# Kernel optimization log

Hardware: AMD Instinct MI355X
Metric: run time of the kernel (lower is better)

## Reference

```python
import jax, jax.numpy as jnp
import numpy as np

N, A, B, K = 100000, 64, 128, 27  # active sites, in/out channels, 3^3 offsets
EPS = 1e-4  # scn BatchNorm default eps
LEAK = 0.0  # leakiness=0 -> ReLU


def bn_lrelu(x, gamma, beta):
    # training-mode BN over active sites, fused leaky relu
    mu = x.mean(0)
    var = x.var(0)
    xh = (x - mu) * jax.lax.rsqrt(var + EPS) * gamma + beta
    return jnp.where(xh > 0, xh, LEAK * xh)


def subconv(f, nbr, mask, W):
    # submanifold conv via rulebook: f [N,Cin], nbr [N,K], mask [N,K], W [K,Cin,Cout]
    out = jnp.zeros((f.shape[0], W.shape[2]), f.dtype)
    for k in range(W.shape[0]):  # fixed small set of kernel offsets
        g = jnp.where(mask[:, k:k + 1], f[nbr[:, k]], jnp.zeros((), f.dtype))
        out = out + g @ W[k]
    return out


def setup_inputs() -> dict:
    key = jax.random.key(0)
    ks = jax.random.split(key, 8)
    feat = jax.random.normal(ks[0], (N, A), jnp.float32)
    nbr = jax.random.randint(ks[1], (N, K), 0, N, jnp.int32)
    mask = jax.random.randint(ks[2], (N, K), 0, 2, jnp.int32).astype(bool)
    # self-connection at center offset is always valid in submanifold conv
    center = K // 2
    nbr = nbr.at[:, center].set(jnp.arange(N, dtype=jnp.int32))
    mask = mask.at[:, center].set(True)
    s1 = 1.0 / np.sqrt(K * A)
    s2 = 1.0 / np.sqrt(K * B)
    W1 = jax.random.normal(ks[3], (K, A, B), jnp.float32) * s1
    W2 = jax.random.normal(ks[4], (K, B, B), jnp.float32) * s2
    Wnin = jax.random.normal(ks[5], (A, B), jnp.float32) / np.sqrt(A)
    gamma1 = jnp.ones((A,), jnp.float32)
    beta1 = jnp.zeros((A,), jnp.float32)
    gamma2 = jnp.ones((B,), jnp.float32)
    beta2 = jnp.zeros((B,), jnp.float32)
    return {"feat": feat, "gamma1": gamma1, "beta1": beta1, "W1": W1,
            "gamma2": gamma2, "beta2": beta2, "W2": W2, "Wnin": Wnin,
            "nbr": nbr, "mask": mask}


def reference(feat, gamma1, beta1, W1, gamma2, beta2, W2, Wnin, nbr, mask):
    y1 = feat @ Wnin  # NetworkInNetwork shortcut (a != b)
    h = bn_lrelu(feat, gamma1, beta1)
    h = subconv(h, nbr, mask, W1)
    h = bn_lrelu(h, gamma2, beta2)
    y2 = subconv(h, nbr, mask, W2)
    return y1 + y2  # add_feature_planes
```

## Files before the change

### kernel.cpp

```cpp
#include <hip/hip_runtime.h>
#include <stdint.h>

#define CA 64
#define CB 128
#define KOFF 27
#define BN_EPS 1e-4f

typedef short bf16x8 __attribute__((ext_vector_type(8)));
typedef float f32x4 __attribute__((ext_vector_type(4)));
typedef unsigned int u32x4 __attribute__((ext_vector_type(4)));
typedef unsigned short u16x4 __attribute__((ext_vector_type(4)));

__device__ __forceinline__ unsigned short f2bf(float f) {
  union { float f; uint32_t u; } c; c.f = f;
  uint32_t u = c.u;
  return (unsigned short)((u + 0x7FFFu + ((u >> 16) & 1u)) >> 16);
}

__device__ __forceinline__ void barrier_lds() {
  asm volatile("s_waitcnt lgkmcnt(0)\n\ts_barrier" ::: "memory");
}

__global__ void detect_mask_k(const unsigned char* __restrict__ m, int* flag) {
  unsigned v = 0;
  for (int i = threadIdx.x; i < 4096; i += 256)
    if (i & 3) v |= m[i];
  if (v) atomicOr(flag, 1);
}

__global__ void pack_mask_k(const void* __restrict__ mp, const int* __restrict__ flag,
                            uint32_t* __restrict__ bits, int n) {
  int i = blockIdx.x * blockDim.x + threadIdx.x;
  if (i >= n) return;
  uint32_t b = 0;
  if (*flag) {
    const unsigned char* m = (const unsigned char*)mp + (size_t)i * KOFF;
    for (int k = 0; k < KOFF; k++) b |= (m[k] ? 1u : 0u) << k;
  } else {
    const int* m = (const int*)mp + (size_t)i * KOFF;
    for (int k = 0; k < KOFF; k++) b |= (m[k] ? 1u : 0u) << k;
  }
  bits[i] = b;
}

__global__ void transpose_all_k(const float* __restrict__ W1, const float* __restrict__ W2,
                                const float* __restrict__ Wnin,
                                unsigned short* __restrict__ w1t, unsigned short* __restrict__ w2t,
                                unsigned short* __restrict__ wnt) {
  const int t1 = KOFF * CA * CB, t2 = KOFF * CB * CB, t3 = CA * CB;
  int idx = blockIdx.x * blockDim.x + threadIdx.x;
  if (idx < t1) {
    int ci = idx % CA; int r = idx / CA; int co = r % CB; int k = r / CB;
    w1t[idx] = f2bf(W1[((size_t)k * CA + ci) * CB + co]);
  } else if (idx < t1 + t2) {
    int j = idx - t1;
    int ci = j % CB; int r = j / CB; int co = r % CB; int k = r / CB;
    w2t[j] = f2bf(W2[((size_t)k * CB + ci) * CB + co]);
  } else if (idx < t1 + t2 + t3) {
    int j = idx - t1 - t2;
    int ci = j % CA; int co = j / CA;
    wnt[j] = f2bf(Wnin[(size_t)ci * CB + co]);
  }
}

template<int C>
__global__ void col_stats_k(const float* __restrict__ x, int n, float* __restrict__ sums) {
  __shared__ float ssum[C], ssq[C];
  int t = threadIdx.x;
  for (int i = t; i < C; i += 256) { ssum[i] = 0.f; ssq[i] = 0.f; }
  __syncthreads();
  const int c = t % C;
  const int rpb = 256 / C;
  float s = 0.f, q = 0.f;
  for (int r = blockIdx.x * rpb + t / C; r < n; r += gridDim.x * rpb) {
    float v = x[(size_t)r * C + c];
    s += v; q += v * v;
  }
  atomicAdd(&ssum[c], s);
  atomicAdd(&ssq[c], q);
  __syncthreads();
  for (int i = t; i < C; i += 256) {
    atomicAdd(&sums[i], ssum[i]);
    atomicAdd(&sums[C + i], ssq[i]);
  }
}

template<int C>
__global__ void bn_finalize_k(const float* __restrict__ sums, const float* __restrict__ gamma,
                              const float* __restrict__ beta, float* __restrict__ sc, int n) {
  int c = threadIdx.x;
  if (c >= C) return;
  float inv_n = 1.f / (float)n;
  float mean = sums[c] * inv_n;
  float var = sums[C + c] * inv_n - mean * mean;
  float rstd = rsqrtf(var + BN_EPS);
  float scale = gamma[c] * rstd;
  sc[c] = scale;
  sc[C + c] = beta[c] - mean * scale;
}

template<int C, bool RAW>
__global__ void bn_apply_k(const float* __restrict__ x, const float* __restrict__ sc,
                           unsigned short* __restrict__ h, unsigned short* __restrict__ raw,
                           int total) {
  int idx = (blockIdx.x * blockDim.x + threadIdx.x) * 4;
  if (idx >= total) return;
  f32x4 v = *(const f32x4*)&x[idx];
  int c0 = idx % C;
  u16x4 ho, ro;
#pragma unroll
  for (int j = 0; j < 4; j++) {
    float s = sc[c0 + j], b = sc[C + c0 + j];
    float hv = fmaxf(v[j] * s + b, 0.f);
    ho[j] = f2bf(hv);
    if (RAW) ro[j] = f2bf(v[j]);
  }
  *(u16x4*)&h[idx] = ho;
  if (RAW) *(u16x4*)&raw[idx] = ro;
}

template<int CIN, bool FUSE, bool STATS>
__launch_bounds__(256, 4)
__global__ void conv_k(const unsigned short* __restrict__ hin,
                       const unsigned short* __restrict__ wt,
                       const int* __restrict__ nbr,
                       const uint32_t* __restrict__ mbits,
                       const unsigned short* __restrict__ fbraw,
                       const unsigned short* __restrict__ wnt,
                       float* __restrict__ out, float* __restrict__ sums, int n) {
  constexpr int TR = 64;
  constexpr int NKS = CIN / 32;
  constexpr int CH = CIN / 8;
  constexpr int RPP = 256 / CH;
  constexpr int NP = TR / RPP;

  __shared__ alignas(16) unsigned short tile[2][TR * CIN];
  __shared__ int lnbr[TR * KOFF];
  __shared__ uint32_t lmb[TR];

  const int t = threadIdx.x;
  const int rowbase = blockIdx.x * TR;
  const int nrows = min(TR, n - rowbase);

  for (int i = t; i < nrows * KOFF; i += 256)
    lnbr[i] = nbr[(size_t)rowbase * KOFF + i] * (CIN * 2);
  if (t < TR) lmb[t] = (t < nrows) ? mbits[rowbase + t] : 0u;
  barrier_lds();

  const int lane = t & 63;
  const int wave = t >> 6;
  const int l16 = lane & 15;
  const int quad = lane >> 4;
  const int colbase = wave * 32;
  const int c16 = t % CH;
  const int grow = t / CH;
  const int boff0 = (colbase + l16) * CIN + quad * 8;
  const int boff1 = boff0 + 16 * CIN;

  int toff[NP]; int pnb[NP]; uint32_t pmb[NP];
#pragma unroll
  for (int p = 0; p < NP; p++) {
    int r = p * RPP + grow;
    toff[p] = r * CIN + ((c16 ^ (r & (CH - 1))) * 8);
    pnb[p] = r * KOFF;
    pmb[p] = lmb[r];
  }

  f32x4 acc[4][2];
#pragma unroll
  for (int i = 0; i < 4; i++) { acc[i][0] = f32x4{0,0,0,0}; acc[i][1] = f32x4{0,0,0,0}; }

  bf16x8 bfr[2 * NKS];
  u32x4 gr[2][NP];
  u32x4 g0[NP];

#define LOADB(kk, dst)                                                         \
  {                                                                            \
    const unsigned short* wk = wt + (size_t)(kk) * (CB * CIN);                 \
    _Pragma("unroll")                                                          \
    for (int ks = 0; ks < NKS; ks++) {                                         \
      dst[2 * ks]     = *(const bf16x8*)&wk[boff0 + ks * 32];                  \
      dst[2 * ks + 1] = *(const bf16x8*)&wk[boff1 + ks * 32];                  \
    }                                                                          \
  }

#define GATHER(kk, dst)                                                        \
  {                                                                            \
    _Pragma("unroll")                                                          \
    for (int p = 0; p < NP; p++) {                                             \
      u32x4 v = {0, 0, 0, 0};                                                  \
      if ((pmb[p] >> (kk)) & 1u)                                               \
        v = *(const u32x4*)((const char*)hin +                                 \
                            (size_t)(unsigned)lnbr[pnb[p] + (kk)] + c16 * 16); \
      dst[p] = v;                                                              \
    }                                                                          \
  }

#define STAGE(buf, src)                                                        \
  {                                                                            \
    _Pragma("unroll")                                                          \
    for (int p = 0; p < NP; p++) *(u32x4*)&tile[buf][toff[p]] = src[p];        \
  }

#define MMA(buf)                                                               \
  {                                                                            \
    _Pragma("unroll")                                                          \
    for (int ks = 0; ks < NKS; ks++) {                                         \
      _Pragma("unroll")                                                        \
      for (int rt = 0; rt < 4; rt++) {                                         \
        int row = rt * 16 + l16;                                               \
        bf16x8 a = *(const bf16x8*)&tile[buf][row * CIN +                      \
                      (((ks * 4 + quad) ^ (row & (CH - 1))) * 8)];             \
        acc[rt][0] = __builtin_amdgcn_mfma_f32_16x16x32_bf16(a, bfr[2 * ks],     acc[rt][0], 0, 0, 0); \
        acc[rt][1] = __builtin_amdgcn_mfma_f32_16x16x32_bf16(a, bfr[2 * ks + 1], acc[rt][1], 0, 0, 0); \
      }                                                                        \
    }                                                                          \
  }

  LOADB(0, bfr);
  GATHER(0, g0);

  if constexpr (FUSE) {
#pragma unroll
    for (int ks = 0; ks < CA / 32; ks++) {
      bf16x8 b0 = *(const bf16x8*)&wnt[(colbase + l16) * CA + ks * 32 + quad * 8];
      bf16x8 b1 = *(const bf16x8*)&wnt[(colbase + 16 + l16) * CA + ks * 32 + quad * 8];
#pragma unroll
      for (int rt = 0; rt < 4; rt++) {
        int r = rt * 16 + l16;
        bf16x8 a = bf16x8{0, 0, 0, 0, 0, 0, 0, 0};
        if (r < nrows)
          a = *(const bf16x8*)&fbraw[(size_t)(rowbase + r) * CA + ks * 32 + quad * 8];
        acc[rt][0] = __builtin_amdgcn_mfma_f32_16x16x32_bf16(a, b0, acc[rt][0], 0, 0, 0);
        acc[rt][1] = __builtin_amdgcn_mfma_f32_16x16x32_bf16(a, b1, acc[rt][1], 0, 0, 0);
      }
    }
  }

  STAGE(0, g0);
  GATHER(1, gr[0]);
  GATHER(2, gr[1]);
  barrier_lds();

#pragma unroll
  for (int k = 0; k < KOFF; k++) {
    const int cur = k & 1, nxt = cur ^ 1;
    MMA(cur);
    if (k + 1 < KOFF) {
      LOADB(k + 1, bfr);
      STAGE(nxt, gr[cur]);
      if (k + 3 < KOFF) GATHER(k + 3, gr[cur]);
      barrier_lds();
    }
  }
#undef LOADB
#undef GATHER
#undef STAGE
#undef MMA

#pragma unroll
  for (int rt = 0; rt < 4; rt++) {
#pragma unroll
    for (int ct = 0; ct < 2; ct++) {
#pragma unroll
      for (int i = 0; i < 4; i++) {
        int r = rt * 16 + quad * 4 + i;
        if (r < nrows) {
          int c = colbase + ct * 16 + l16;
          out[(size_t)(rowbase + r) * CB + c] = acc[rt][ct][i];
        }
      }
    }
  }

  if constexpr (STATS) {
#pragma unroll
    for (int ct = 0; ct < 2; ct++) {
      float s = 0.f, q = 0.f;
#pragma unroll
      for (int rt = 0; rt < 4; rt++)
#pragma unroll
        for (int i = 0; i < 4; i++) { float v = acc[rt][ct][i]; s += v; q += v * v; }
      s += __shfl_xor(s, 16); s += __shfl_xor(s, 32);
      q += __shfl_xor(q, 16); q += __shfl_xor(q, 32);
      if (quad == 0) {
        int cch = colbase + ct * 16 + l16;
        atomicAdd(&sums[cch], s);
        atomicAdd(&sums[CB + cch], q);
      }
    }
  }
}

extern "C" void kernel_launch(void* const* d_in, const int* in_sizes, int n_in,
                              void* d_out, int out_size, void* d_ws, size_t ws_size,
                              hipStream_t stream) {
  const float* feat   = (const float*)d_in[0];
  const float* gamma1 = (const float*)d_in[1];
  const float* beta1  = (const float*)d_in[2];
  const float* W1     = (const float*)d_in[3];
  const float* gamma2 = (const float*)d_in[4];
  const float* beta2  = (const float*)d_in[5];
  const float* W2     = (const float*)d_in[6];
  const float* Wnin   = (const float*)d_in[7];
  const int*   nbr    = (const int*)d_in[8];
  const void*  mask   = d_in[9];
  float* out = (float*)d_out;

  const int n = in_sizes[0] / CA;

  char* ws = (char*)d_ws;
  size_t off = 0;
  auto alloc = [&](size_t bytes) { size_t p = off; off += (bytes + 255) & ~(size_t)255; return p; };
  int*            flag  = (int*)           (ws + alloc(256));
  float*          sums1 = (float*)         (ws + alloc(2 * CA * 4));
  float*          sums2 = (float*)         (ws + alloc(2 * CB * 4));
  float*          sc1   = (float*)         (ws + alloc(2 * CA * 4));
  float*          sc2   = (float*)         (ws + alloc(2 * CB * 4));
  uint32_t*       mbits = (uint32_t*)      (ws + alloc((size_t)n * 4));
  unsigned short* fb    = (unsigned short*)(ws + alloc((size_t)n * CA * 2));
  unsigned short* hb1   = (unsigned short*)(ws + alloc((size_t)n * CA * 2));
  float*          out1  = (float*)         (ws + alloc((size_t)n * CB * 4));
  unsigned short* hb2   = (unsigned short*)(ws + alloc((size_t)n * CB * 2));
  unsigned short* w1t   = (unsigned short*)(ws + alloc((size_t)KOFF * CB * CA * 2));
  unsigned short* w2t   = (unsigned short*)(ws + alloc((size_t)KOFF * CB * CB * 2));
  unsigned short* wnt   = (unsigned short*)(ws + alloc((size_t)CB * CA * 2));

  hipMemsetAsync(d_ws, 0, 1792, stream);

  detect_mask_k<<<1, 256, 0, stream>>>((const unsigned char*)mask, flag);
  pack_mask_k<<<(n + 255) / 256, 256, 0, stream>>>(mask, flag, mbits, n);

  {
    int tot = KOFF * CA * CB + KOFF * CB * CB + CA * CB;
    transpose_all_k<<<(tot + 255) / 256, 256, 0, stream>>>(W1, W2, Wnin, w1t, w2t, wnt);
  }

  col_stats_k<CA><<<256, 256, 0, stream>>>(feat, n, sums1);
  bn_finalize_k<CA><<<1, CA, 0, stream>>>(sums1, gamma1, beta1, sc1, n);
  bn_apply_k<CA, true><<<(n * CA / 4 + 255) / 256, 256, 0, stream>>>(feat, sc1, hb1, fb, n * CA);

  conv_k<CA, false, true><<<(n + 63) / 64, 256, 0, stream>>>(hb1, w1t, nbr, mbits, nullptr, nullptr, out1, sums2, n);

  bn_finalize_k<CB><<<1, CB, 0, stream>>>(sums2, gamma2, beta2, sc2, n);
  bn_apply_k<CB, false><<<(n * CB / 4 + 255) / 256, 256, 0, stream>>>(out1, sc2, hb2, nullptr, n * CB);

  conv_k<CB, true, false><<<(n + 63) / 64, 256, 0, stream>>>(hb2, w2t, nbr, mbits, fb, wnt, out, nullptr, n);
}
```

Measured before the change: 536.4 us.

## Gather conv A-operands directly from global into registers, dropping LDS staging

Replaces the LDS double-buffered gather tile and barriers with per-lane direct global loads of the neighbour rows in MFMA operand layout. The neighbour indices are read from global per offset and a two-deep register pipeline covers latency. The launch-bounds occupancy hint is removed. This eliminates LDS writes, reads and block-wide barriers. In exchange each wave issues its own redundant gathers, four waves reloading the same rows, so L2 traffic rises, and register pressure may change occupancy.

```diff
diff --git a/kernel.cpp b/kernel.cpp
--- a/kernel.cpp
+++ b/kernel.cpp
@@ -15,10 +15,6 @@
   union { float f; uint32_t u; } c; c.f = f;
   uint32_t u = c.u;
   return (unsigned short)((u + 0x7FFFu + ((u >> 16) & 1u)) >> 16);
-}
-
-__device__ __forceinline__ void barrier_lds() {
-  asm volatile("s_waitcnt lgkmcnt(0)\n\ts_barrier" ::: "memory");
 }
 
 __global__ void detect_mask_k(const unsigned char* __restrict__ m, int* flag) {
@@ -120,7 +116,7 @@
 }
 
 template<int CIN, bool FUSE, bool STATS>
-__launch_bounds__(256, 4)
+__launch_bounds__(256)
 __global__ void conv_k(const unsigned short* __restrict__ hin,
                        const unsigned short* __restrict__ wt,
                        const int* __restrict__ nbr,
@@ -130,95 +126,79 @@
                        float* __restrict__ out, float* __restrict__ sums, int n) {
   constexpr int TR = 64;
   constexpr int NKS = CIN / 32;
-  constexpr int CH = CIN / 8;
-  constexpr int RPP = 256 / CH;
-  constexpr int NP = TR / RPP;
-
-  __shared__ alignas(16) unsigned short tile[2][TR * CIN];
-  __shared__ int lnbr[TR * KOFF];
-  __shared__ uint32_t lmb[TR];
+  constexpr int NG = KOFF * NKS;
 
   const int t = threadIdx.x;
-  const int rowbase = blockIdx.x * TR;
-  const int nrows = min(TR, n - rowbase);
-
-  for (int i = t; i < nrows * KOFF; i += 256)
-    lnbr[i] = nbr[(size_t)rowbase * KOFF + i] * (CIN * 2);
-  if (t < TR) lmb[t] = (t < nrows) ? mbits[rowbase + t] : 0u;
-  barrier_lds();
-
   const int lane = t & 63;
   const int wave = t >> 6;
   const int l16 = lane & 15;
   const int quad = lane >> 4;
   const int colbase = wave * 32;
-  const int c16 = t % CH;
-  const int grow = t / CH;
-  const int boff0 = (colbase + l16) * CIN + quad * 8;
-  const int boff1 = boff0 + 16 * CIN;
-
-  int toff[NP]; int pnb[NP]; uint32_t pmb[NP];
-#pragma unroll
-  for (int p = 0; p < NP; p++) {
-    int r = p * RPP + grow;
-    toff[p] = r * CIN + ((c16 ^ (r & (CH - 1))) * 8);
-    pnb[p] = r * KOFF;
-    pmb[p] = lmb[r];
-  }
+  const int rowbase = blockIdx.x * TR;
+  const int nrows = min(TR, n - rowbase);
+
+  uint32_t pm[4];
+  int nbo[4];
+#pragma unroll
+  for (int rt = 0; rt < 4; rt++) {
+    int r = rt * 16 + l16;
+    bool ok = r < nrows;
+    pm[rt] = ok ? mbits[rowbase + r] : 0u;
+    nbo[rt] = (ok ? (rowbase + r) : rowbase) * KOFF;
+  }
+
+  const char* hq  = (const char*)hin + quad * 16;
+  const char* wq0 = (const char*)wt + ((colbase + l16) * CIN + quad * 8) * 2;
+  const char* wq1 = wq0 + 16 * CIN * 2;
 
   f32x4 acc[4][2];
 #pragma unroll
   for (int i = 0; i < 4; i++) { acc[i][0] = f32x4{0,0,0,0}; acc[i][1] = f32x4{0,0,0,0}; }
 
-  bf16x8 bfr[2 * NKS];
-  u32x4 gr[2][NP];
-  u32x4 g0[NP];
-
-#define LOADB(kk, dst)                                                         \
-  {                                                                            \
-    const unsigned short* wk = wt + (size_t)(kk) * (CB * CIN);                 \
+  int nb0[4], nb1[4], nb2[4];
+  bf16x8 aA[4], aB[4];
+  bf16x8 bA0, bA1, bB0, bB1;
+
+#define LDNB_BODY(kk, nb)                                                      \
+    { _Pragma("unroll")                                                        \
+      for (int rt = 0; rt < 4; rt++) nb[rt] = nbr[nbo[rt] + (kk)]; }
+#define LDNB(kk) do {                                                          \
+    if (((kk) % 3) == 0)      LDNB_BODY(kk, nb0)                               \
+    else if (((kk) % 3) == 1) LDNB_BODY(kk, nb1)                               \
+    else                      LDNB_BODY(kk, nb2)                               \
+  } while (0)
+
+#define LOADA_BODY(kk, ks, nb, a)                                              \
+    { _Pragma("unroll")                                                        \
+      for (int rt = 0; rt < 4; rt++) {                                         \
+        bf16x8 v = bf16x8{0, 0, 0, 0, 0, 0, 0, 0};                             \
+        if ((pm[rt] >> (kk)) & 1u)                                             \
+          v = *(const bf16x8*)(hq +                                            \
+                (size_t)((unsigned)nb[rt] * (unsigned)(CIN * 2)) + (ks) * 64); \
+        a[rt] = v; } }
+#define LOADA(kk, ks, a) do {                                                  \
+    if (((kk) % 3) == 0)      LOADA_BODY(kk, ks, nb0, a)                       \
+    else if (((kk) % 3) == 1) LOADA_BODY(kk, ks, nb1, a)                       \
+    else                      LOADA_BODY(kk, ks, nb2, a)                       \
+  } while (0)
+
+#define LOADW(kk, ks, b0, b1) do {                                             \
+    int woff = (kk) * (CB * CIN * 2) + (ks) * 64;                              \
+    b0 = *(const bf16x8*)(wq0 + woff);                                         \
+    b1 = *(const bf16x8*)(wq1 + woff);                                         \
+  } while (0)
+
+#define MMA8(a, b0, b1) do {                                                   \
     _Pragma("unroll")                                                          \
-    for (int ks = 0; ks < NKS; ks++) {                                         \
-      dst[2 * ks]     = *(const bf16x8*)&wk[boff0 + ks * 32];                  \
-      dst[2 * ks + 1] = *(const bf16x8*)&wk[boff1 + ks * 32];                  \
-    }                                                                          \
-  }
-
-#define GATHER(kk, dst)                                                        \
-  {                                                                            \
-    _Pragma("unroll")                                                          \
-    for (int p = 0; p < NP; p++) {                                             \
-      u32x4 v = {0, 0, 0, 0};                                                  \
-      if ((pmb[p] >> (kk)) & 1u)                                               \
-        v = *(const u32x4*)((const char*)hin +                                 \
-                            (size_t)(unsigned)lnbr[pnb[p] + (kk)] + c16 * 16); \
-      dst[p] = v;                                                              \
-    }                                                                          \
-  }
-
-#define STAGE(buf, src)                                                        \
-  {                                                                            \
-    _Pragma("unroll")                                                          \
-    for (int p = 0; p < NP; p++) *(u32x4*)&tile[buf][toff[p]] = src[p];        \
-  }
-
-#define MMA(buf)                                                               \
-  {                                                                            \
-    _Pragma("unroll")                                                          \
-    for (int ks = 0; ks < NKS; ks++) {                                         \
-      _Pragma("unroll")                                                        \
-      for (int rt = 0; rt < 4; rt++) {                                         \
-        int row = rt * 16 + l16;                                               \
-        bf16x8 a = *(const bf16x8*)&tile[buf][row * CIN +                      \
-                      (((ks * 4 + quad) ^ (row & (CH - 1))) * 8)];             \
-        acc[rt][0] = __builtin_amdgcn_mfma_f32_16x16x32_bf16(a, bfr[2 * ks],     acc[rt][0], 0, 0, 0); \
-        acc[rt][1] = __builtin_amdgcn_mfma_f32_16x16x32_bf16(a, bfr[2 * ks + 1], acc[rt][1], 0, 0, 0); \
-      }                                                                        \
-    }                                                                          \
-  }
-
-  LOADB(0, bfr);
-  GATHER(0, g0);
+    for (int rt = 0; rt < 4; rt++) {                                           \
+      acc[rt][0] = __builtin_amdgcn_mfma_f32_16x16x32_bf16(a[rt], b0, acc[rt][0], 0, 0, 0); \
+      acc[rt][1] = __builtin_amdgcn_mfma_f32_16x16x32_bf16(a[rt], b1, acc[rt][1], 0, 0, 0); \
+    } } while (0)
+
+  LDNB(0);
+  LDNB(1);
+  LOADA(0, 0, aA); LOADW(0, 0, bA0, bA1);
+  LOADA(0, 1, aB); LOADW(0, 1, bB0, bB1);
 
   if constexpr (FUSE) {
 #pragma unroll
@@ -237,26 +217,25 @@
     }
   }
 
-  STAGE(0, g0);
-  GATHER(1, gr[0]);
-  GATHER(2, gr[1]);
-  barrier_lds();
-
-#pragma unroll
-  for (int k = 0; k < KOFF; k++) {
-    const int cur = k & 1, nxt = cur ^ 1;
-    MMA(cur);
-    if (k + 1 < KOFF) {
-      LOADB(k + 1, bfr);
-      STAGE(nxt, gr[cur]);
-      if (k + 3 < KOFF) GATHER(k + 3, gr[cur]);
-      barrier_lds();
+#pragma unroll
+  for (int g = 0; g < NG; g++) {
+    const int k = g / NKS, ks = g % NKS;
+    (void)ks;
+    if ((g & 1) == 0) MMA8(aA, bA0, bA1); else MMA8(aB, bB0, bB1);
+    if ((g % NKS) == 0 && k + 2 < KOFF) LDNB(k + 2);
+    const int g2 = g + 2;
+    if (g2 < NG) {
+      const int k2 = g2 / NKS, ks2 = g2 % NKS;
+      if ((g & 1) == 0) { LOADA(k2, ks2, aA); LOADW(k2, ks2, bA0, bA1); }
+      else              { LOADA(k2, ks2, aB); LOADW(k2, ks2, bB0, bB1); }
     }
   }
-#undef LOADB
-#undef GATHER
-#undef STAGE
-#undef MMA
+#undef LDNB_BODY
+#undef LDNB
+#undef LOADA_BODY
+#undef LOADA
+#undef LOADW
+#undef MMA8
 
 #pragma unroll
   for (int rt = 0; rt < 4; rt++) {
```

New measurement: 851.8 us. 58.8% more time.

## Gather neighbor rows directly into LDS with global_load_lds DMA

Applied to the files above, without the earlier changes.

Replaces the register-staged gather (global load to VGPRs, then store to LDS) with global_load_lds direct-to-LDS transfers. Masked-off neighbors read from a zeroed scratch page. Neighbor indices are loaded per offset from global memory into registers instead of being prestaged in LDS. The swizzle moves into the source address, and barriers now wait on vmcnt so the next offset's DMA overlaps the current MMA. This removes VGPR traffic and the LDS prologue, but leaves only one offset of prefetch depth instead of two, and drops the launch-bounds occupancy hint.

```diff
diff --git a/kernel.cpp b/kernel.cpp
--- a/kernel.cpp
+++ b/kernel.cpp
@@ -15,10 +15,6 @@
   union { float f; uint32_t u; } c; c.f = f;
   uint32_t u = c.u;
   return (unsigned short)((u + 0x7FFFu + ((u >> 16) & 1u)) >> 16);
-}
-
-__device__ __forceinline__ void barrier_lds() {
-  asm volatile("s_waitcnt lgkmcnt(0)\n\ts_barrier" ::: "memory");
 }
 
 __global__ void detect_mask_k(const unsigned char* __restrict__ m, int* flag) {
@@ -120,59 +116,72 @@
 }
 
 template<int CIN, bool FUSE, bool STATS>
-__launch_bounds__(256, 4)
+__launch_bounds__(256)
 __global__ void conv_k(const unsigned short* __restrict__ hin,
                        const unsigned short* __restrict__ wt,
                        const int* __restrict__ nbr,
                        const uint32_t* __restrict__ mbits,
                        const unsigned short* __restrict__ fbraw,
                        const unsigned short* __restrict__ wnt,
+                       const char* __restrict__ zpage,
                        float* __restrict__ out, float* __restrict__ sums, int n) {
   constexpr int TR = 64;
   constexpr int NKS = CIN / 32;
   constexpr int CH = CIN / 8;
   constexpr int RPP = 256 / CH;
+  constexpr int RPW = 64 / CH;
   constexpr int NP = TR / RPP;
 
   __shared__ alignas(16) unsigned short tile[2][TR * CIN];
-  __shared__ int lnbr[TR * KOFF];
-  __shared__ uint32_t lmb[TR];
 
   const int t = threadIdx.x;
-  const int rowbase = blockIdx.x * TR;
-  const int nrows = min(TR, n - rowbase);
-
-  for (int i = t; i < nrows * KOFF; i += 256)
-    lnbr[i] = nbr[(size_t)rowbase * KOFF + i] * (CIN * 2);
-  if (t < TR) lmb[t] = (t < nrows) ? mbits[rowbase + t] : 0u;
-  barrier_lds();
-
   const int lane = t & 63;
   const int wave = t >> 6;
   const int l16 = lane & 15;
   const int quad = lane >> 4;
   const int colbase = wave * 32;
+  const int rowbase = blockIdx.x * TR;
+  const int nrows = min(TR, n - rowbase);
+
   const int c16 = t % CH;
   const int grow = t / CH;
+  const char* hsrc = (const char*)hin + (c16 ^ (grow & (CH - 1))) * 16;
+  const int wvrow = wave * RPW;
+
+  uint32_t pm[NP]; int nbro[NP];
+#pragma unroll
+  for (int p = 0; p < NP; p++) {
+    int rg = rowbase + p * RPP + grow;
+    pm[p] = (rg < n) ? mbits[rg] : 0u;
+    nbro[p] = min(rg, n - 1) * KOFF;
+  }
+
   const int boff0 = (colbase + l16) * CIN + quad * 8;
   const int boff1 = boff0 + 16 * CIN;
 
-  int toff[NP]; int pnb[NP]; uint32_t pmb[NP];
-#pragma unroll
-  for (int p = 0; p < NP; p++) {
-    int r = p * RPP + grow;
-    toff[p] = r * CIN + ((c16 ^ (r & (CH - 1))) * 8);
-    pnb[p] = r * KOFF;
-    pmb[p] = lmb[r];
-  }
-
   f32x4 acc[4][2];
 #pragma unroll
   for (int i = 0; i < 4; i++) { acc[i][0] = f32x4{0,0,0,0}; acc[i][1] = f32x4{0,0,0,0}; }
 
   bf16x8 bfr[2 * NKS];
-  u32x4 gr[2][NP];
-  u32x4 g0[NP];
+  int nbE[NP], nbO[NP];
+
+#define NBLOAD(kk, nb)                                                         \
+  { _Pragma("unroll")                                                          \
+    for (int p = 0; p < NP; p++) nb[p] = nbr[nbro[p] + (kk)]; }
+
+#define DMASTAGE(kk, buf, nb)                                                  \
+  { _Pragma("unroll")                                                          \
+    for (int p = 0; p < NP; p++) {                                             \
+      const char* g = ((pm[p] >> (kk)) & 1u)                                   \
+          ? hsrc + (size_t)((unsigned)nb[p] * (unsigned)(CIN * 2))             \
+          : zpage;                                                             \
+      __builtin_amdgcn_global_load_lds(                                        \
+          (const __attribute__((address_space(1))) void*)g,                    \
+          (__attribute__((address_space(3))) void*)                            \
+              &tile[buf][(p * RPP + wvrow) * CIN],                             \
+          16, 0, 0);                                                           \
+    } }
 
 #define LOADB(kk, dst)                                                         \
   {                                                                            \
@@ -182,24 +191,6 @@
       dst[2 * ks]     = *(const bf16x8*)&wk[boff0 + ks * 32];                  \
       dst[2 * ks + 1] = *(const bf16x8*)&wk[boff1 + ks * 32];                  \
     }                                                                          \
-  }
-
-#define GATHER(kk, dst)                                                        \
-  {                                                                            \
-    _Pragma("unroll")                                                          \
-    for (int p = 0; p < NP; p++) {                                             \
-      u32x4 v = {0, 0, 0, 0};                                                  \
-      if ((pmb[p] >> (kk)) & 1u)                                               \
-        v = *(const u32x4*)((const char*)hin +                                 \
-                            (size_t)(unsigned)lnbr[pnb[p] + (kk)] + c16 * 16); \
-      dst[p] = v;                                                              \
-    }                                                                          \
-  }
-
-#define STAGE(buf, src)                                                        \
-  {                                                                            \
-    _Pragma("unroll")                                                          \
-    for (int p = 0; p < NP; p++) *(u32x4*)&tile[buf][toff[p]] = src[p];        \
   }
 
 #define MMA(buf)                                                               \
@@ -217,8 +208,14 @@
     }                                                                          \
   }
 
-  LOADB(0, bfr);
-  GATHER(0, g0);
+#define WAITBAR()                                                              \
+  asm volatile("s_waitcnt vmcnt(%0) lgkmcnt(0)\n\ts_barrier"                   \
+               :: "i"(2 * NKS) : "memory")
+
+  NBLOAD(0, nbE);
+  DMASTAGE(0, 0, nbE);
+  NBLOAD(1, nbO);
+  __builtin_amdgcn_sched_barrier(0);
 
   if constexpr (FUSE) {
 #pragma unroll
@@ -237,26 +234,30 @@
     }
   }
 
-  STAGE(0, g0);
-  GATHER(1, gr[0]);
-  GATHER(2, gr[1]);
-  barrier_lds();
+  LOADB(0, bfr);
+  WAITBAR();
 
 #pragma unroll
   for (int k = 0; k < KOFF; k++) {
     const int cur = k & 1, nxt = cur ^ 1;
+    if (k + 1 < KOFF) {
+      if (((k + 1) & 1) == 0) DMASTAGE(k + 1, nxt, nbE) else DMASTAGE(k + 1, nxt, nbO);
+      if (k + 2 < KOFF) {
+        if (((k + 2) & 1) == 0) NBLOAD(k + 2, nbE) else NBLOAD(k + 2, nbO);
+      }
+      __builtin_amdgcn_sched_barrier(0);
+    }
     MMA(cur);
     if (k + 1 < KOFF) {
       LOADB(k + 1, bfr);
-      STAGE(nxt, gr[cur]);
-      if (k + 3 < KOFF) GATHER(k + 3, gr[cur]);
-      barrier_lds();
-    }
-  }
+      WAITBAR();
+    }
+  }
+#undef NBLOAD
+#undef DMASTAGE
 #undef LOADB
-#undef GATHER
-#undef STAGE
 #undef MMA
+#undef WAITBAR
 
 #pragma unroll
   for (int rt = 0; rt < 4; rt++) {
@@ -313,6 +314,7 @@
   size_t off = 0;
   auto alloc = [&](size_t bytes) { size_t p = off; off += (bytes + 255) & ~(size_t)255; return p; };
   int*            flag  = (int*)           (ws + alloc(256));
+  char*           zpage = (char*)          (ws + alloc(256));
   float*          sums1 = (float*)         (ws + alloc(2 * CA * 4));
   float*          sums2 = (float*)         (ws + alloc(2 * CB * 4));
   float*          sc1   = (float*)         (ws + alloc(2 * CA * 4));
@@ -326,7 +328,7 @@
   unsigned short* w2t   = (unsigned short*)(ws + alloc((size_t)KOFF * CB * CB * 2));
   unsigned short* wnt   = (unsigned short*)(ws + alloc((size_t)CB * CA * 2));
 
-  hipMemsetAsync(d_ws, 0, 1792, stream);
+  hipMemsetAsync(d_ws, 0, 2048, stream);
 
   detect_mask_k<<<1, 256, 0, stream>>>((const unsigned char*)mask, flag);
   pack_mask_k<<<(n + 255) / 256, 256, 0, stream>>>(mask, flag, mbits, n);
@@ -340,10 +342,10 @@
   bn_finalize_k<CA><<<1, CA, 0, stream>>>(sums1, gamma1, beta1, sc1, n);
   bn_apply_k<CA, true><<<(n * CA / 4 + 255) / 256, 256, 0, stream>>>(feat, sc1, hb1, fb, n * CA);
 
-  conv_k<CA, false, true><<<(n + 63) / 64, 256, 0, stream>>>(hb1, w1t, nbr, mbits, nullptr, nullptr, out1, sums2, n);
+  conv_k<CA, false, true><<<(n + 63) / 64, 256, 0, stream>>>(hb1, w1t, nbr, mbits, nullptr, nullptr, zpage, out1, sums2, n);
 
   bn_finalize_k<CB><<<1, CB, 0, stream>>>(sums2, gamma2, beta2, sc2, n);
   bn_apply_k<CB, false><<<(n * CB / 4 + 255) / 256, 256, 0, stream>>>(out1, sc2, hb2, nullptr, n * CB);
 
-  conv_k<CB, true, false><<<(n + 63) / 64, 256, 0, stream>>>(hb2, w2t, nbr, mbits, fb, wnt, out, nullptr, n);
-}
+  conv_k<CB, true, false><<<(n + 63) / 64, 256, 0, stream>>>(hb2, w2t, nbr, mbits, fb, wnt, zpage, out, nullptr, n);
+}
```

Measured after the change: 513.7 us. 1.04x faster.
